# Kernel tuning notes

Hardware: AMD Instinct MI355X
Metric: run time of the kernel (lower is better)

Reference implementation:

```python
import jax, jax.numpy as jnp
import numpy as np
from jax import lax

NUM_BLOCKS = 8
BLOCK = 4  # hidden_size 32 // num_blocks 8
LAMBDA = 0.01  # sparsity_threshold
BN_EPS = 1e-5


def _bn(x, gamma, beta):
    # training-mode BatchNorm2d over (N, H, W) per channel
    mean = jnp.mean(x, axis=(0, 2, 3), keepdims=True)
    var = jnp.var(x, axis=(0, 2, 3), keepdims=True)
    return gamma[None, :, None, None] * (x - mean) * lax.rsqrt(var + BN_EPS) + beta[None, :, None, None]


def _softshrink(x, lam):
    return jnp.where(x > lam, x - lam, jnp.where(x < -lam, x + lam, jnp.zeros_like(x)))


def _afno(x, w1, b1, w2, b2):
    # AFNO2D_channelfirst: rfft2 -> block-diagonal complex 2-layer MLP -> softshrink
    # -> multiply with original spectrum -> irfft2 -> residual add
    B, C, H, W = x.shape
    bias = x
    xf = jnp.fft.rfft2(x, axes=(2, 3), norm="ortho")          # [B, C, H, W//2+1] complex
    orig = xf
    Wf = xf.shape[-1]
    xb = xf.reshape(B, NUM_BLOCKS, BLOCK, H, Wf)
    xr, xi = jnp.real(xb), jnp.imag(xb)
    # layer 1 (complex block matmul + bias + ReLU)
    o1r = jax.nn.relu(jnp.einsum('bkihw,kio->bkohw', xr, w1[0])
                      - jnp.einsum('bkihw,kio->bkohw', xi, w1[1])
                      + b1[0][None, :, :, None, None])
    o1i = jax.nn.relu(jnp.einsum('bkihw,kio->bkohw', xi, w1[0])
                      + jnp.einsum('bkihw,kio->bkohw', xr, w1[1])
                      + b1[1][None, :, :, None, None])
    # layer 2
    o2r = (jnp.einsum('bkihw,kio->bkohw', o1r, w2[0])
           - jnp.einsum('bkihw,kio->bkohw', o1i, w2[1])
           + b2[0][None, :, :, None, None])
    o2i = (jnp.einsum('bkihw,kio->bkohw', o1i, w2[0])
           + jnp.einsum('bkihw,kio->bkohw', o1r, w2[1])
           + b2[1][None, :, :, None, None])
    o2r = _softshrink(o2r, LAMBDA)
    o2i = _softshrink(o2i, LAMBDA)
    z = (o2r + 1j * o2i).reshape(B, C, H, Wf)
    z = z * orig                                              # spectral gating by original spectrum
    out = jnp.fft.irfft2(z, s=(H, W), axes=(2, 3), norm="ortho")
    return out + bias


def setup_inputs() -> dict:
    key = jax.random.key(0)
    ks = jax.random.split(key, 6)
    return {
        "x": jax.random.normal(ks[0], (4, 32, 512, 512), jnp.float32),
        "conv_w": jax.random.normal(ks[1], (32, 32, 3, 3), jnp.float32) * 0.05,
        "conv_b": jnp.zeros((32,), jnp.float32),
        "bn1_gamma": jnp.ones((32,), jnp.float32),
        "bn1_beta": jnp.zeros((32,), jnp.float32),
        "w1": jax.random.normal(ks[2], (2, NUM_BLOCKS, BLOCK, BLOCK), jnp.float32) * 0.02,
        "b1": jax.random.normal(ks[3], (2, NUM_BLOCKS, BLOCK), jnp.float32) * 0.02,
        "w2": jax.random.normal(ks[4], (2, NUM_BLOCKS, BLOCK, BLOCK), jnp.float32) * 0.02,
        "b2": jax.random.normal(ks[5], (2, NUM_BLOCKS, BLOCK), jnp.float32) * 0.02,
        "bn2_gamma": jnp.ones((32,), jnp.float32),
        "bn2_beta": jnp.zeros((32,), jnp.float32),
    }


def reference(x, conv_w, conv_b, bn1_gamma, bn1_beta, w1, b1, w2, b2, bn2_gamma, bn2_beta):
    # conv1 = Conv3x3(norm=True, act=True): conv 3x3 pad 1 + BN + ReLU
    y = lax.conv_general_dilated(x, conv_w, (1, 1), ((1, 1), (1, 1)),
                                 dimension_numbers=('NCHW', 'OIHW', 'NCHW'))
    y = y + conv_b[None, :, None, None]
    y = jax.nn.relu(_bn(y, bn1_gamma, bn1_beta))
    fo = _afno(y, w1, b1, w2, b2)
    fo = _bn(fo, bn2_gamma, bn2_beta)
    return jax.nn.relu(y + fo)
```

## Files before the change

kernel.cpp:

```cpp
#include <hip/hip_runtime.h>

#define WF 257
#define LAM 0.01f
#define ROWH 540
#define LPH(i) ((i) + (((i)>>6)<<2))

#define WSYNC() do { asm volatile("" ::: "memory"); __builtin_amdgcn_wave_barrier(); asm volatile("" ::: "memory"); } while(0)

typedef __attribute__((ext_vector_type(8))) short short8;
typedef __attribute__((ext_vector_type(4))) float f32x4;
typedef __attribute__((ext_vector_type(2))) __fp16 h2v;
typedef __attribute__((ext_vector_type(8))) __fp16 h8;

union UH8 { uint4 u; h8 h; };

__device__ __forceinline__ ushort f2bf(float f){
    unsigned u = __float_as_uint(f);
    unsigned r = (u + 0x7fffu + ((u >> 16) & 1u)) >> 16;
    return (ushort)r;
}
__device__ __forceinline__ float bf2f(ushort u){ return __uint_as_float((uint)u << 16); }
__device__ __forceinline__ uint packbf(float a, float b){
    return (uint)f2bf(a) | ((uint)f2bf(b) << 16);
}
__device__ __forceinline__ float2 unpackbf(uint u){
    return make_float2(__uint_as_float(u << 16), __uint_as_float(u & 0xffff0000u));
}
__device__ __forceinline__ uint packh(float a, float b){
    h2v h;
    h[0] = (__fp16)a;
    h[1] = (__fp16)b;
    return *(uint*)&h;
}
__device__ __forceinline__ uint packh2(float2 v){ return packh(v.x, v.y); }
__device__ __forceinline__ float2 unph(uint u){
    h2v h = *(h2v*)&u;
    return make_float2((float)h[0], (float)h[1]);
}

__device__ __forceinline__ float2 cmul(float2 a, float2 b){
    return make_float2(a.x*b.x - a.y*b.y, a.x*b.y + a.y*b.x);
}
__device__ __forceinline__ float2 cadd(float2 a, float2 b){ return make_float2(a.x+b.x, a.y+b.y); }
__device__ __forceinline__ float2 csub(float2 a, float2 b){ return make_float2(a.x-b.x, a.y-b.y); }

template<int NTHREADS>
__device__ __forceinline__ void ld_tw(float2* tw, const float2* __restrict__ twg, int tid){
    for (int t = tid; t < 256; t += NTHREADS)
        ((float4*)tw)[t] = ((const float4*)twg)[t];
}

template<bool INV>
__device__ __forceinline__ float2 twz(const float2* tw, int idx){
    float2 w = tw[idx];
    if (INV) w.y = -w.y;
    return w;
}

template<bool INV>
__device__ __forceinline__ void dft8(float2 v[8]) {
    const float R = 0.70710678118654752f;
    float2 y0=v[0], y1=v[4], y2=v[2], y3=v[6], y4=v[1], y5=v[5], y6=v[3], y7=v[7];
    float2 t;
    t=y1; y1=csub(y0,t); y0=cadd(y0,t);
    t=y3; y3=csub(y2,t); y2=cadd(y2,t);
    t=y5; y5=csub(y4,t); y4=cadd(y4,t);
    t=y7; y7=csub(y6,t); y6=cadd(y6,t);
    t=y2; y2=csub(y0,t); y0=cadd(y0,t);
    t = INV ? make_float2(-y3.y, y3.x) : make_float2(y3.y, -y3.x);
    y3=csub(y1,t); y1=cadd(y1,t);
    t=y6; y6=csub(y4,t); y4=cadd(y4,t);
    t = INV ? make_float2(-y7.y, y7.x) : make_float2(y7.y, -y7.x);
    y7=csub(y5,t); y5=cadd(y5,t);
    t=y4; y4=csub(y0,t); y0=cadd(y0,t);
    { float2 w8 = INV ? make_float2(R, R) : make_float2(R,-R);
      t=cmul(y5,w8); y5=csub(y1,t); y1=cadd(y1,t); }
    t = INV ? make_float2(-y6.y, y6.x) : make_float2(y6.y, -y6.x);
    y6=csub(y2,t); y2=cadd(y2,t);
    { float2 w8 = INV ? make_float2(-R, R) : make_float2(-R,-R);
      t=cmul(y7,w8); y7=csub(y3,t); y3=cadd(y3,t); }
    v[0]=y0; v[1]=y1; v[2]=y2; v[3]=y3; v[4]=y4; v[5]=y5; v[6]=y6; v[7]=y7;
}

__device__ __forceinline__ void oct_write(uint* drow, int l, const float2 v[8]){
    uint* p = drow + LPH(8*l);
    *(uint4*)p       = make_uint4(packh2(v[0]), packh2(v[1]), packh2(v[2]), packh2(v[3]));
    *(uint4*)(p + 4) = make_uint4(packh2(v[4]), packh2(v[5]), packh2(v[6]), packh2(v[7]));
}

__device__ __forceinline__ void oct_gather(const uint* drow, int o0, float2 v[8]){
    const uint* b = drow + LPH(o0);
    #pragma unroll
    for (int q = 0; q < 8; ++q) v[q] = unph(b[68*q]);
}

template<bool INV>
__device__ __forceinline__ void fft_wave12(uint* drow, const float2* tw, int l)
{
    WSYNC();
    {
        int a = l&7, m = l>>3;
        uint* b = drow + 68*m + a;
        float2 v[8];
        v[0] = unph(b[0]);
        #pragma unroll
        for (int j = 1; j < 8; ++j)
            v[j] = cmul(unph(b[8*j]), twz<INV>(tw, 8*a*j));
        dft8<INV>(v);
        #pragma unroll
        for (int j = 0; j < 8; ++j) b[8*j] = packh2(v[j]);
    }
    WSYNC();
    {
        uint* b = drow + l;
        float2 v[8];
        v[0] = unph(b[0]);
        #pragma unroll
        for (int q = 1; q < 8; ++q)
            v[q] = cmul(unph(b[68*q]), twz<INV>(tw, (l*q)&511));
        dft8<INV>(v);
        #pragma unroll
        for (int q = 0; q < 8; ++q) b[68*q] = packh2(v[q]);
    }
    WSYNC();
}

__global__ void k_twiddle(float2* __restrict__ twg){
    int t = blockIdx.x*256 + threadIdx.x;
    if (t < 512) {
        float s, c;
        sincosf((float)t * (-6.2831853071795864769f/512.0f), &s, &c);
        twg[t] = make_float2(c, s);
    }
}

__device__ __forceinline__ float2 twf(int idx){
    float s, c;
    sincosf((float)(idx & 511) * (-6.2831853071795864769f/512.0f), &s, &c);
    return make_float2(c, s);
}

__global__ void k_mfrag(uint4* __restrict__ fA, uint4* __restrict__ fB,
                        uint4* __restrict__ fG, uint4* __restrict__ fC)
{
    const int lane = threadIdx.x;
    const int bx = blockIdx.x;
    const int l15 = lane & 15;
    const int kb = (lane >> 4) * 8;
    if (bx < 2) {
        const int mt = bx;
        const int m = mt*16 + l15;
        uint ur[4], ui[4], un[4];
        for (int p = 0; p < 4; ++p) {
            float2 t0 = twf(16*m*(kb + 2*p));
            float2 t1 = twf(16*m*(kb + 2*p+1));
            ur[p] = packh(t0.x, t1.x);
            ui[p] = packh(t0.y, t1.y);
            un[p] = ui[p] ^ 0x80008000u;
        }
        fA[(lane*2 + mt)*3 + 0] = make_uint4(ur[0],ur[1],ur[2],ur[3]);
        fA[(lane*2 + mt)*3 + 1] = make_uint4(ui[0],ui[1],ui[2],ui[3]);
        fA[(lane*2 + mt)*3 + 2] = make_uint4(un[0],un[1],un[2],un[3]);
    } else if (bx < 34) {
        const int k2 = bx - 2;
        uint ar[4]={0,0,0,0}, ai[4]={0,0,0,0}, an[4]={0,0,0,0};
        if (lane < 32) {
            const int kk = k2 + 32*l15;
            for (int p = 0; p < 4; ++p) {
                float2 t0 = twf((kb + 2*p)*kk);
                float2 t1 = twf((kb + 2*p+1)*kk);
                ar[p] = packh(t0.x, t1.x);
                ai[p] = packh(t0.y, t1.y);
                an[p] = ai[p] ^ 0x80008000u;
            }
        }
        fB[(lane*32 + k2)*3 + 0] = make_uint4(ar[0],ar[1],ar[2],ar[3]);
        fB[(lane*32 + k2)*3 + 1] = make_uint4(ai[0],ai[1],ai[2],ai[3]);
        fB[(lane*32 + k2)*3 + 2] = make_uint4(an[0],an[1],an[2],an[3]);
    } else if (bx == 34) {
        uint gr[4]={0,0,0,0}, gi[4]={0,0,0,0}, gn[4]={0,0,0,0};
        if (lane < 32) {
            for (int p = 0; p < 4; ++p) {
                float2 t0 = twf(32*(kb + 2*p)*l15);
                float2 t1 = twf(32*(kb + 2*p+1)*l15);
                gr[p] = packh(t0.x, t1.x);
                gi[p] = packh(-t0.y, -t1.y);
                gn[p] = gi[p] ^ 0x80008000u;
            }
        }
        fG[lane*3 + 0] = make_uint4(gr[0],gr[1],gr[2],gr[3]);
        fG[lane*3 + 1] = make_uint4(gi[0],gi[1],gi[2],gi[3]);
        fG[lane*3 + 2] = make_uint4(gn[0],gn[1],gn[2],gn[3]);
    } else {
        const int t = bx - 35;
        const int n1 = t >> 1, mt = t & 1;
        const int hh = n1 + 16*(mt*16 + l15);
        uint cr[4], ci[4], cn[4];
        for (int p = 0; p < 4; ++p) {
            float2 t0 = twf(hh*(kb + 2*p));
            float2 t1 = twf(hh*(kb + 2*p+1));
            cr[p] = packh(t0.x, t1.x);
            ci[p] = packh(-t0.y, -t1.y);
            cn[p] = ci[p] ^ 0x80008000u;
        }
        fC[((lane*16 + n1)*2 + mt)*3 + 0] = make_uint4(cr[0],cr[1],cr[2],cr[3]);
        fC[((lane*16 + n1)*2 + mt)*3 + 1] = make_uint4(ci[0],ci[1],ci[2],ci[3]);
        fC[((lane*16 + n1)*2 + mt)*3 + 2] = make_uint4(cn[0],cn[1],cn[2],cn[3]);
    }
}

__global__ void k_wprep(const float* __restrict__ w, ushort* __restrict__ wtp){
    int i = blockIdx.x*256 + threadIdx.x;
    if (i < 9216) {
        int j = i & 7, l = (i>>3) & 63, m = (i>>9) & 1, tap = i >> 10;
        int co = m*16 + (l & 15), ci = ((l>>4)&3)*8 + j;
        wtp[i] = f2bf(w[(co*32 + ci)*9 + tap]);
    }
}

__global__ __launch_bounds__(256) void k_transpose(const float* __restrict__ x, ushort* __restrict__ xt){
    __shared__ ushort tl[64][36];
    const int tid = threadIdx.x;
    const int w0 = blockIdx.x*64, h = blockIdx.y, b = blockIdx.z;
    #pragma unroll
    for (int it = 0; it < 8; ++it) {
        int i = it*256 + tid, c = i >> 6, ww = i & 63;
        tl[ww][c] = f2bf(x[(((size_t)b*32 + c)*512 + h)*512 + w0 + ww]);
    }
    __syncthreads();
    const int ww = tid >> 2, c0 = (tid & 3) * 8;
    uint4 v;
    v.x = *(const uint*)&tl[ww][c0+0];
    v.y = *(const uint*)&tl[ww][c0+2];
    v.z = *(const uint*)&tl[ww][c0+4];
    v.w = *(const uint*)&tl[ww][c0+6];
    *(uint4*)(xt + ((((size_t)b*512 + h)*512 + w0 + ww)*32 + c0)) = v;
}

__global__ __launch_bounds__(256) void k_conv_mfma(
    const ushort* __restrict__ xt, const ushort* __restrict__ wtp,
    const float* __restrict__ bias, ushort* __restrict__ out, float* __restrict__ stats)
{
    __shared__ float sred[64];
    const int tid = threadIdx.x;
    const int wid = tid >> 6, lane = tid & 63;
    const int h = blockIdx.y*4 + wid;
    const int w0 = blockIdx.x*64;
    const int b = blockIdx.z;

    short8 wa[9][2];
    #pragma unroll
    for (int tap = 0; tap < 9; ++tap)
        #pragma unroll
        for (int m = 0; m < 2; ++m)
            wa[tap][m] = *reinterpret_cast<const short8*>(wtp + ((tap*2 + m)*64 + lane)*8);

    f32x4 acc[2][4];
    #pragma unroll
    for (int m = 0; m < 2; ++m)
        #pragma unroll
        for (int n = 0; n < 4; ++n)
            acc[m][n] = (f32x4){0.f, 0.f, 0.f, 0.f};

    const int c0 = ((lane >> 4) & 3) * 8;
    const int pw = w0 + (lane & 15);
    const size_t ibase = (size_t)b * 512 * 512;

    #pragma unroll
    for (int dy = -1; dy <= 1; ++dy) {
        const int hh = h + dy;
        const bool hok = (unsigned)hh < 512u;
        #pragma unroll
        for (int dx = -1; dx <= 1; ++dx) {
            const int tap = (dy+1)*3 + (dx+1);
            short8 bfr[4];
            #pragma unroll
            for (int n = 0; n < 4; ++n) {
                const int ww = pw + n*16 + dx;
                short8 v = {0,0,0,0,0,0,0,0};
                if (hok && (unsigned)ww < 512u)
                    v = *reinterpret_cast<const short8*>(xt + ((ibase + (size_t)hh*512 + ww)*32 + c0));
                bfr[n] = v;
            }
            #pragma unroll
            for (int m = 0; m < 2; ++m)
                #pragma unroll
                for (int n = 0; n < 4; ++n)
                    acc[m][n] = __builtin_amdgcn_mfma_f32_16x16x32_bf16(wa[tap][m], bfr[n], acc[m][n], 0, 0, 0);
        }
    }

    if (tid < 64) sred[tid] = 0.f;
    __syncthreads();

    float bv[2][4];
    #pragma unroll
    for (int m = 0; m < 2; ++m)
        #pragma unroll
        for (int r = 0; r < 4; ++r)
            bv[m][r] = bias[m*16 + ((lane>>4)&3)*4 + r];

    float s8[8], q8[8];
    #pragma unroll
    for (int i = 0; i < 8; ++i) { s8[i] = 0.f; q8[i] = 0.f; }

    #pragma unroll
    for (int m = 0; m < 2; ++m) {
        #pragma unroll
        for (int n = 0; n < 4; ++n) {
            #pragma unroll
            for (int r = 0; r < 4; ++r) {
                const int co = m*16 + ((lane>>4)&3)*4 + r;
                const int ww = w0 + n*16 + (lane & 15);
                float val = acc[m][n][r] + bv[m][r];
                out[(((size_t)b*32 + co)*512 + h)*512 + ww] = f2bf(val);
                s8[m*4+r] += val;
                q8[m*4+r] += val*val;
            }
        }
    }
    #pragma unroll
    for (int i = 0; i < 8; ++i) {
        #pragma unroll
        for (int off = 1; off < 16; off <<= 1) {
            s8[i] += __shfl_xor(s8[i], off, 64);
            q8[i] += __shfl_xor(q8[i], off, 64);
        }
    }
    if ((lane & 15) == 0) {
        #pragma unroll
        for (int m = 0; m < 2; ++m)
            #pragma unroll
            for (int r = 0; r < 4; ++r) {
                const int co = m*16 + ((lane>>4)&3)*4 + r;
                atomicAdd(&sred[co], s8[m*4+r]);
                atomicAdd(&sred[32+co], q8[m*4+r]);
            }
    }
    __syncthreads();
    if (tid < 64) {
        int bin = (blockIdx.y*8 + blockIdx.x + blockIdx.z) & 63;
        atomicAdd(&stats[bin*64 + tid], sred[tid]);
    }
}

__global__ void k_finalize(const float* __restrict__ stats, int nbins, const float* __restrict__ g,
                           const float* __restrict__ bta, float* __restrict__ bnp)
{
    int c = threadIdx.x;
    if (c < 32) {
        float s = 0.f, q = 0.f;
        for (int i = 0; i < nbins; ++i) { s += stats[i*64 + c]; q += stats[i*64 + 32 + c]; }
        const float inv_n = 1.f/1048576.f;
        float mean = s * inv_n;
        float var  = q * inv_n - mean*mean;
        float sc = g[c] * rsqrtf(var + 1e-5f);
        bnp[c] = sc;
        bnp[32+c] = bta[c] - mean*sc;
    }
}

__global__ void k_finalize2(const float* __restrict__ ystats, const float* __restrict__ sstats,
                            const float* __restrict__ g, const float* __restrict__ bta,
                            float* __restrict__ bnp2)
{
    int c = threadIdx.x;
    if (c < 32) {
        float Sy = 0.f, Sy2 = 0.f, Sgg = 0.f, Sgu = 0.f, Sg0 = 0.f;
        for (int i = 0; i < 64; ++i){ Sy  += ystats[i*64 + c]; Sy2 += ystats[i*64 + 32 + c]; }
        for (int i = 0; i < 32; ++i){ Sgg += sstats[i*96 + c]; Sgu += sstats[i*96 + 32 + c]; Sg0 += sstats[i*96 + 64 + c]; }
        const float inv_n = 1.f/1048576.f;
        float Sfo  = Sg0 + Sy;
        float Sfo2 = Sgg*(1.f/512.f) + Sgu*(2.f/512.f) + Sy2;
        float mean = Sfo*inv_n;
        float var  = Sfo2*inv_n - mean*mean;
        float sc = g[c]*rsqrtf(var + 1e-5f);
        bnp2[c] = sc;
        bnp2[32+c] = bta[c] - mean*sc;
    }
}

__global__ __launch_bounds__(512) void k_rowfft_fwd(
    const ushort* __restrict__ cvo, const float* __restrict__ bnp,
    const float2* __restrict__ twg, uint* __restrict__ spec, float* __restrict__ ystats)
{
    __shared__ float2 tw[512];
    __shared__ uint d[8*ROWH];
    const int tid = threadIdx.x;
    const int h0 = blockIdx.x * 16;
    const int bc = blockIdx.y;
    const int c = bc & 31;
    ld_tw<512>(tw, twg, tid);
    __syncthreads();
    const float s1 = bnp[c], t1 = bnp[32+c];
    const int row = tid >> 6, l = tid & 63;
    const int o0 = ((l&7)<<3) | (l>>3);
    uint* drow = d + row*ROWH;
    const ushort* rp0 = cvo + ((size_t)bc*512 + h0 + 2*row)*512 + o0;
    const ushort* rp1 = rp0 + 512;
    float ls = 0.f, lsq = 0.f;
    float2 v[8];
    #pragma unroll
    for (int q = 0; q < 8; ++q) {
        float y0 = fmaxf(fmaf(bf2f(rp0[64*q]), s1, t1), 0.f);
        float y1 = fmaxf(fmaf(bf2f(rp1[64*q]), s1, t1), 0.f);
        ls += y0 + y1; lsq += y0*y0 + y1*y1;
        v[q] = make_float2(y0, y1);
    }
    dft8<false>(v);
    oct_write(drow, l, v);
    fft_wave12<false>(drow, tw, l);
    __syncthreads();
    for (int i = tid; i < 8*WF; i += 512) {
        int p = i & 7, w = i >> 3;
        float2 Z  = unph(d[p*ROWH + LPH(w)]);
        float2 Zm = unph(d[p*ROWH + LPH((512 - w) & 511)]);
        float x1r = 0.5f*(Z.x + Zm.x), x1i = 0.5f*(Z.y - Zm.y);
        float x2r = 0.5f*(Z.y + Zm.y), x2i = 0.5f*(Zm.x - Z.x);
        uint2 pk;
        pk.x = packbf(x1r, x1i);
        pk.y = packbf(x2r, x2i);
        *(uint2*)(spec + ((size_t)bc*WF + w)*512 + h0 + 2*p) = pk;
    }
    #pragma unroll
    for (int off = 32; off; off >>= 1){ ls += __shfl_down(ls, off, 64); lsq += __shfl_down(lsq, off, 64); }
    if (l == 0) {
        int bin = ((blockIdx.x << 3) + row) & 63;
        atomicAdd(&ystats[bin*64 + c], ls);
        atomicAdd(&ystats[bin*64 + 32 + c], lsq);
    }
}

__global__ __launch_bounds__(512) void k_colfft(uint* __restrict__ spec,
    const float* __restrict__ w1, const float* __restrict__ b1,
    const float* __restrict__ w2, const float* __restrict__ b2,
    const uint4* __restrict__ fA, const uint4* __restrict__ fB,
    const uint4* __restrict__ fG, const uint4* __restrict__ fC,
    float* __restrict__ sstats)
{
    __shared__ uint sl[32*513];
    __shared__ float wl[640];
    const int tid = threadIdx.x;
    const int lane = tid & 63, wv = tid >> 6;
    const int w = blockIdx.x, b = blockIdx.y;
    const int l15 = lane & 15, lq = lane >> 4;
    const int kb = lq * 8;

    if (tid < 128) {
        int g = tid >> 4, j = tid & 15;
        wl[g*80 + j]      = w1[g*16 + j];
        wl[g*80 + 16 + j] = w1[128 + g*16 + j];
        wl[g*80 + 32 + j] = w2[g*16 + j];
        wl[g*80 + 48 + j] = w2[128 + g*16 + j];
    } else if (tid < 160) {
        int t2 = tid - 128, g = t2 >> 2, o = t2 & 3;
        wl[g*80 + 64 + o] = b1[g*4 + o];
        wl[g*80 + 68 + o] = b1[32 + g*4 + o];
        wl[g*80 + 72 + o] = b2[g*4 + o];
        wl[g*80 + 76 + o] = b2[32 + g*4 + o];
    }
    const size_t gbase = ((size_t)b*32*WF + w) * 512;
    #pragma unroll 4
    for (int c = 0; c < 32; ++c) {
        float2 u = unpackbf(spec[gbase + (size_t)c*(WF*512) + tid]);
        sl[c*513 + tid] = packh(u.x*(1.f/512.f), u.y*(1.f/512.f));
    }
    __syncthreads();

    {
        h8 Fr[2], Fi[2], nFi[2];
        #pragma unroll
        for (int mt = 0; mt < 2; ++mt) {
            UH8 a; a.u = fA[(lane*2 + mt)*3 + 0]; Fr[mt]=a.h;
            UH8 bb; bb.u = fA[(lane*2 + mt)*3 + 1]; Fi[mt]=bb.h;
            UH8 cc; cc.u = fA[(lane*2 + mt)*3 + 2]; nFi[mt]=cc.h;
        }
        #pragma unroll
        for (int s = 0; s < 2; ++s) {
            const int n1 = wv*2 + s;
            h8 Br[2], Bi[2];
            #pragma unroll
            for (int nt = 0; nt < 2; ++nt) {
                const int base = (nt*16 + l15)*513 + n1;
                uint dd[8];
                #pragma unroll
                for (int j = 0; j < 8; ++j) dd[j] = sl[base + 16*(kb + j)];
                uint br[4], bi[4];
                #pragma unroll
                for (int p = 0; p < 4; ++p) {
                    br[p] = (dd[2*p] & 0xffffu) | (dd[2*p+1] << 16);
                    bi[p] = (dd[2*p] >> 16) | (dd[2*p+1] & 0xffff0000u);
                }
                UH8 t1_; t1_.u = make_uint4(br[0],br[1],br[2],br[3]); Br[nt]=t1_.h;
                UH8 t2_; t2_.u = make_uint4(bi[0],bi[1],bi[2],bi[3]); Bi[nt]=t2_.h;
            }
            __builtin_amdgcn_s_setprio(1);
            #pragma unroll
            for (int mt = 0; mt < 2; ++mt)
            #pragma unroll
            for (int nt = 0; nt < 2; ++nt) {
                f32x4 yr = {0.f,0.f,0.f,0.f}, yi = {0.f,0.f,0.f,0.f};
                yr = __builtin_amdgcn_mfma_f32_16x16x32_f16(Fr[mt], Br[nt], yr, 0,0,0);
                yr = __builtin_amdgcn_mfma_f32_16x16x32_f16(nFi[mt], Bi[nt], yr, 0,0,0);
                yi = __builtin_amdgcn_mfma_f32_16x16x32_f16(Fr[mt], Bi[nt], yi, 0,0,0);
                yi = __builtin_amdgcn_mfma_f32_16x16x32_f16(Fi[mt], Br[nt], yi, 0,0,0);
                const int cw = (nt*16 + l15)*513 + n1;
                #pragma unroll
                for (int r = 0; r < 4; ++r)
                    sl[cw + 16*(mt*16 + lq*4 + r)] = packh(yr[r], yi[r]);
            }
            __builtin_amdgcn_s_setprio(0);
        }
    }
    __syncthreads();

    #pragma unroll
    for (int s = 0; s < 4; ++s) {
        const int k2 = wv*4 + s;
        h8 Ar, Ai, nAi;
        {
            UH8 a; a.u = fB[(lane*32 + k2)*3 + 0]; Ar=a.h;
            UH8 bb; bb.u = fB[(lane*32 + k2)*3 + 1]; Ai=bb.h;
            UH8 cc; cc.u = fB[(lane*32 + k2)*3 + 2]; nAi=cc.h;
        }
        #pragma unroll
        for (int ct = 0; ct < 2; ++ct) {
            const int cb2 = (ct*16 + l15)*513 + 16*k2;
            h8 Br, Bi;
            {
                uint dd[8] = {0,0,0,0,0,0,0,0};
                if (lane < 32) {
                    #pragma unroll
                    for (int j = 0; j < 8; ++j) dd[j] = sl[cb2 + kb + j];
                }
                uint br[4], bi[4];
                #pragma unroll
                for (int p = 0; p < 4; ++p) {
                    br[p] = (dd[2*p] & 0xffffu) | (dd[2*p+1] << 16);
                    bi[p] = (dd[2*p] >> 16) | (dd[2*p+1] & 0xffff0000u);
                }
                UH8 t1_; t1_.u = make_uint4(br[0],br[1],br[2],br[3]); Br=t1_.h;
                UH8 t2_; t2_.u = make_uint4(bi[0],bi[1],bi[2],bi[3]); Bi=t2_.h;
            }
            __builtin_amdgcn_s_setprio(1);
            f32x4 xr = {0.f,0.f,0.f,0.f}, xi = {0.f,0.f,0.f,0.f};
            xr = __builtin_amdgcn_mfma_f32_16x16x32_f16(Ar, Br, xr, 0,0,0);
            xr = __builtin_amdgcn_mfma_f32_16x16x32_f16(nAi, Bi, xr, 0,0,0);
            xi = __builtin_amdgcn_mfma_f32_16x16x32_f16(Ar, Bi, xi, 0,0,0);
            xi = __builtin_amdgcn_mfma_f32_16x16x32_f16(Ai, Br, xi, 0,0,0);
            __builtin_amdgcn_s_setprio(0);
            #pragma unroll
            for (int r = 0; r < 4; ++r)
                sl[cb2 + lq*4 + r] = packh(xr[r], xi[r]);
        }
    }
    __syncthreads();

    #pragma unroll
    for (int g = 0; g < 8; ++g) {
        const float* wk = wl + g*80;
        float xr[4], xi[4];
        #pragma unroll
        for (int i = 0; i < 4; ++i) {
            float2 v = unph(sl[(4*g+i)*513 + tid]);
            xr[i] = v.x; xi[i] = v.y;
        }
        float o1r[4], o1i[4];
        #pragma unroll
        for (int o = 0; o < 4; ++o) {
            float sr = wk[64+o], si = wk[68+o];
            #pragma unroll
            for (int i = 0; i < 4; ++i) {
                float wr = wk[i*4+o], wi = wk[16 + i*4+o];
                sr += xr[i]*wr - xi[i]*wi;
                si += xi[i]*wr + xr[i]*wi;
            }
            o1r[o] = fmaxf(sr, 0.f);
            o1i[o] = fmaxf(si, 0.f);
        }
        #pragma unroll
        for (int o = 0; o < 4; ++o) {
            float sr = wk[72+o], si = wk[76+o];
            #pragma unroll
            for (int i = 0; i < 4; ++i) {
                float wr = wk[32 + i*4+o], wi = wk[48 + i*4+o];
                sr += o1r[i]*wr - o1i[i]*wi;
                si += o1i[i]*wr + o1r[i]*wi;
            }
            sr = (sr > LAM) ? sr - LAM : ((sr < -LAM) ? sr + LAM : 0.f);
            si = (si > LAM) ? si - LAM : ((si < -LAM) ? si + LAM : 0.f);
            sl[(4*g+o)*513 + tid] = packh(sr*xr[o] - si*xi[o], sr*xi[o] + si*xr[o]);
        }
    }
    __syncthreads();

    {
        h8 Gr, Gi, nGi;
        {
            UH8 a; a.u = fG[lane*3 + 0]; Gr=a.h;
            UH8 bb; bb.u = fG[lane*3 + 1]; Gi=bb.h;
            UH8 cc; cc.u = fG[lane*3 + 2]; nGi=cc.h;
        }
        #pragma unroll
        for (int s = 0; s < 4; ++s) {
            const int k2 = wv*4 + s;
            #pragma unroll
            for (int ct = 0; ct < 2; ++ct) {
                const int cb2 = (ct*16 + l15)*513 + 16*k2;
                h8 Br, Bi;
                {
                    uint dd[8] = {0,0,0,0,0,0,0,0};
                    if (lane < 32) {
                        #pragma unroll
                        for (int j = 0; j < 8; ++j) dd[j] = sl[cb2 + kb + j];
                    }
                    uint br[4], bi[4];
                    #pragma unroll
                    for (int p = 0; p < 4; ++p) {
                        br[p] = (dd[2*p] & 0xffffu) | (dd[2*p+1] << 16);
                        bi[p] = (dd[2*p] >> 16) | (dd[2*p+1] & 0xffff0000u);
                    }
                    UH8 t1_; t1_.u = make_uint4(br[0],br[1],br[2],br[3]); Br=t1_.h;
                    UH8 t2_; t2_.u = make_uint4(bi[0],bi[1],bi[2],bi[3]); Bi=t2_.h;
                }
                __builtin_amdgcn_s_setprio(1);
                f32x4 yr = {0.f,0.f,0.f,0.f}, yi = {0.f,0.f,0.f,0.f};
                yr = __builtin_amdgcn_mfma_f32_16x16x32_f16(Gr, Br, yr, 0,0,0);
                yr = __builtin_amdgcn_mfma_f32_16x16x32_f16(nGi, Bi, yr, 0,0,0);
                yi = __builtin_amdgcn_mfma_f32_16x16x32_f16(Gr, Bi, yi, 0,0,0);
                yi = __builtin_amdgcn_mfma_f32_16x16x32_f16(Gi, Br, yi, 0,0,0);
                __builtin_amdgcn_s_setprio(0);
                #pragma unroll
                for (int r = 0; r < 4; ++r)
                    sl[cb2 + lq*4 + r] = packh(yr[r], yi[r]);
            }
        }
    }
    __syncthreads();

    #pragma unroll
    for (int s = 0; s < 2; ++s) {
        const int n1 = wv*2 + s;
        h8 Cr[2], Ci[2], nCi[2];
        #pragma unroll
        for (int mt = 0; mt < 2; ++mt) {
            UH8 a; a.u = fC[((lane*16 + n1)*2 + mt)*3 + 0]; Cr[mt]=a.h;
            UH8 bb; bb.u = fC[((lane*16 + n1)*2 + mt)*3 + 1]; Ci[mt]=bb.h;
            UH8 cc; cc.u = fC[((lane*16 + n1)*2 + mt)*3 + 2]; nCi[mt]=cc.h;
        }
        h8 Br[2], Bi[2];
        #pragma unroll
        for (int nt = 0; nt < 2; ++nt) {
            const int base = (nt*16 + l15)*513 + n1;
            uint dd[8];
            #pragma unroll
            for (int j = 0; j < 8; ++j) dd[j] = sl[base + 16*(kb + j)];
            uint br[4], bi[4];
            #pragma unroll
            for (int p = 0; p < 4; ++p) {
                br[p] = (dd[2*p] & 0xffffu) | (dd[2*p+1] << 16);
                bi[p] = (dd[2*p] >> 16) | (dd[2*p+1] & 0xffff0000u);
            }
            UH8 t1_; t1_.u = make_uint4(br[0],br[1],br[2],br[3]); Br[nt]=t1_.h;
            UH8 t2_; t2_.u = make_uint4(bi[0],bi[1],bi[2],bi[3]); Bi[nt]=t2_.h;
        }
        __builtin_amdgcn_s_setprio(1);
        #pragma unroll
        for (int mt = 0; mt < 2; ++mt)
        #pragma unroll
        for (int nt = 0; nt < 2; ++nt) {
            f32x4 xr = {0.f,0.f,0.f,0.f}, xi = {0.f,0.f,0.f,0.f};
            xr = __builtin_amdgcn_mfma_f32_16x16x32_f16(Cr[mt], Br[nt], xr, 0,0,0);
            xr = __builtin_amdgcn_mfma_f32_16x16x32_f16(nCi[mt], Bi[nt], xr, 0,0,0);
            xi = __builtin_amdgcn_mfma_f32_16x16x32_f16(Cr[mt], Bi[nt], xi, 0,0,0);
            xi = __builtin_amdgcn_mfma_f32_16x16x32_f16(Ci[mt], Br[nt], xi, 0,0,0);
            const int cw = (nt*16 + l15)*513 + n1;
            #pragma unroll
            for (int r = 0; r < 4; ++r)
                sl[cw + 16*(mt*16 + lq*4 + r)] = packh(xr[r], xi[r]);
        }
        __builtin_amdgcn_s_setprio(0);
    }
    __syncthreads();

    const bool edge = (w == 0) || (w == 256);
    #pragma unroll
    for (int i = 0; i < 4; ++i) {
        const int c = wv*4 + i;
        const size_t cb = gbase + (size_t)c*(WF*512);
        float fgg = 0.f, fgu = 0.f, fg0 = 0.f;
        #pragma unroll
        for (int it = 0; it < 4; ++it) {
            const int pos = it*128 + 2*lane;
            uint2 dv;
            dv.x = sl[c*513 + pos];
            dv.y = sl[c*513 + pos + 1];
            float2 z0 = unph(dv.x), z1 = unph(dv.y);
            uint2 up = *(const uint2*)(spec + cb + pos);
            float2 u0 = unpackbf(up.x), u1 = unpackbf(up.y);
            uint2 gp;
            gp.x = packbf(z0.x, z0.y);
            gp.y = packbf(z1.x, z1.y);
            *(uint2*)(spec + cb + pos) = gp;
            float2 g0 = unpackbf(gp.x), g1 = unpackbf(gp.y);
            if (edge) {
                fgg += g0.x*g0.x + g1.x*g1.x;
                fgu += g0.x*u0.x + g1.x*u1.x;
                if (w == 0) fg0 += g0.x + g1.x;
            } else {
                fgg += 2.f*(g0.x*g0.x + g0.y*g0.y + g1.x*g1.x + g1.y*g1.y);
                fgu += 2.f*(g0.x*u0.x + g0.y*u0.y + g1.x*u1.x + g1.y*u1.y);
            }
        }
        #pragma unroll
        for (int off = 32; off; off >>= 1){
            fgg += __shfl_down(fgg, off, 64);
            fgu += __shfl_down(fgu, off, 64);
            fg0 += __shfl_down(fg0, off, 64);
        }
        if (lane == 0) {
            const int kk = c >> 2, ch = c & 3;
            const int bin = (w + b*8 + kk) & 31;
            atomicAdd(&sstats[bin*96 + kk*4 + ch], fgg);
            atomicAdd(&sstats[bin*96 + 32 + kk*4 + ch], fgu);
            if (w == 0) atomicAdd(&sstats[bin*96 + 64 + kk*4 + ch], fg0);
        }
    }
}

__global__ __launch_bounds__(512) void k_rowfft_inv(
    const uint* __restrict__ spec, const ushort* __restrict__ cvo,
    const float* __restrict__ bnp, const float* __restrict__ bnp2,
    const float2* __restrict__ twg, float* __restrict__ out)
{
    __shared__ float2 tw[512];
    __shared__ uint d[8*ROWH];
    const int tid = threadIdx.x;
    const int h0 = blockIdx.x * 16;
    const int bc = blockIdx.y;
    const int c = bc & 31;
    ld_tw<512>(tw, twg, tid);
    for (int i = tid; i < 8*WF; i += 512) {
        int p = i & 7, w = i >> 3;
        uint2 pk = *(const uint2*)(spec + ((size_t)bc*WF + w)*512 + h0 + 2*p);
        float2 X1 = unpackbf(pk.x), X2 = unpackbf(pk.y);
        if (w == 0 || w == 256) { X1.y = 0.f; X2.y = 0.f; }
        const float s = 1.f/512.f;
        d[p*ROWH + LPH(w)] = packh((X1.x - X2.y)*s, (X1.y + X2.x)*s);
        if ((unsigned)(w - 1) < 255u)
            d[p*ROWH + LPH(512 - w)] = packh((X1.x + X2.y)*s, (X2.x - X1.y)*s);
    }
    __syncthreads();
    const int row = tid >> 6, l = tid & 63;
    const int o0 = ((l&7)<<3) | (l>>3);
    uint* drow = d + row*ROWH;
    {
        float2 v[8];
        oct_gather(drow, o0, v);
        dft8<true>(v);
        WSYNC();
        oct_write(drow, l, v);
    }
    fft_wave12<true>(drow, tw, l);
    const float s1 = bnp[c],  t1 = bnp[32+c];
    const float s2 = bnp2[c], t2 = bnp2[32+c];
    const size_t gbase = ((size_t)bc*512 + h0 + 2*row)*512;
    #pragma unroll
    for (int q = 0; q < 8; ++q) {
        const int col = q*64 + l;
        float2 v = unph(drow[LPH(col)]);
        float y0 = fmaxf(fmaf(bf2f(cvo[gbase + col]), s1, t1), 0.f);
        float fo0 = v.x + y0;
        out[gbase + col] = fmaxf(y0 + fmaf(fo0, s2, t2), 0.f);
        float y1 = fmaxf(fmaf(bf2f(cvo[gbase + 512 + col]), s1, t1), 0.f);
        float fo1 = v.y + y1;
        out[gbase + 512 + col] = fmaxf(y1 + fmaf(fo1, s2, t2), 0.f);
    }
}

extern "C" void kernel_launch(void* const* d_in, const int* in_sizes, int n_in,
                              void* d_out, int out_size, void* d_ws, size_t ws_size,
                              hipStream_t stream)
{
    const float* x      = (const float*)d_in[0];
    const float* conv_w = (const float*)d_in[1];
    const float* conv_b = (const float*)d_in[2];
    const float* bn1g   = (const float*)d_in[3];
    const float* bn1b   = (const float*)d_in[4];
    const float* w1     = (const float*)d_in[5];
    const float* b1     = (const float*)d_in[6];
    const float* w2     = (const float*)d_in[7];
    const float* b2     = (const float*)d_in[8];
    const float* bn2g   = (const float*)d_in[9];
    const float* bn2b   = (const float*)d_in[10];
    float* out = (float*)d_out;

    char* ws = (char*)d_ws;
    uint*   spec  = (uint*)ws;
    ushort* xt    = (ushort*)ws;
    ushort* cvo   = (ushort*)(ws + 67371008);
    ushort* wtp   = (ushort*)(ws + 67371008 + 67108864);
    float*  stats = (float*)(ws + 67371008 + 67108864 + 18432);
    float* stats1 = stats;
    float* ystats = stats + 4096;
    float* sstats = stats + 8192;
    float* bnp1   = stats + 11264;
    float* bnp2   = stats + 11328;
    float2* twg   = (float2*)(stats + 11392);
    uint4* fA = (uint4*)(stats + 12416);
    uint4* fB = fA + 384;
    uint4* fG = fB + 6144;
    uint4* fC = fG + 192;

    (void)hipMemsetAsync(stats, 0, 11264*sizeof(float), stream);
    k_twiddle<<<2, 256, 0, stream>>>(twg);
    k_mfrag<<<67, 64, 0, stream>>>(fA, fB, fG, fC);
    k_wprep<<<36, 256, 0, stream>>>(conv_w, wtp);
    k_transpose<<<dim3(8,512,4), 256, 0, stream>>>(x, xt);
    k_conv_mfma<<<dim3(8,128,4), 256, 0, stream>>>(xt, wtp, conv_b, cvo, stats1);
    k_finalize<<<1, 64, 0, stream>>>(stats1, 64, bn1g, bn1b, bnp1);
    k_rowfft_fwd<<<dim3(32,128), 512, 0, stream>>>(cvo, bnp1, twg, spec, ystats);
    k_colfft<<<dim3(257,4), 512, 0, stream>>>(spec, w1, b1, w2, b2, fA, fB, fG, fC, sstats);
    k_finalize2<<<1, 64, 0, stream>>>(ystats, sstats, bn2g, bn2b, bnp2);
    k_rowfft_inv<<<dim3(32,128), 512, 0, stream>>>(spec, cvo, bnp1, bnp2, twg, out);
}
```

Measured before the change: 327.7 us.

## Split column FFT kernel across two channel halves to double block count

The column-FFT/spectral-MLP kernel now processes 16 channels per block instead of 32, with a third grid dimension selecting the channel half. Launching 2056 blocks instead of 1028 halves shared memory per block (about 33KB), which should allow more resident blocks per CU and better latency hiding. The cost is that per-block setup such as loading DFT fragments and weights is repeated, and each wave now does less MFMA work per fragment load.

```diff
diff --git a/kernel.cpp b/kernel.cpp
--- a/kernel.cpp
+++ b/kernel.cpp
@@ -438,30 +438,32 @@
     const uint4* __restrict__ fG, const uint4* __restrict__ fC,
     float* __restrict__ sstats)
 {
-    __shared__ uint sl[32*513];
-    __shared__ float wl[640];
+    __shared__ uint sl[16*513];
+    __shared__ float wl[320];
     const int tid = threadIdx.x;
     const int lane = tid & 63, wv = tid >> 6;
-    const int w = blockIdx.x, b = blockIdx.y;
+    const int w = blockIdx.x, b = blockIdx.y, half = blockIdx.z;
     const int l15 = lane & 15, lq = lane >> 4;
     const int kb = lq * 8;
 
-    if (tid < 128) {
+    if (tid < 64) {
         int g = tid >> 4, j = tid & 15;
-        wl[g*80 + j]      = w1[g*16 + j];
-        wl[g*80 + 16 + j] = w1[128 + g*16 + j];
-        wl[g*80 + 32 + j] = w2[g*16 + j];
-        wl[g*80 + 48 + j] = w2[128 + g*16 + j];
-    } else if (tid < 160) {
-        int t2 = tid - 128, g = t2 >> 2, o = t2 & 3;
-        wl[g*80 + 64 + o] = b1[g*4 + o];
-        wl[g*80 + 68 + o] = b1[32 + g*4 + o];
-        wl[g*80 + 72 + o] = b2[g*4 + o];
-        wl[g*80 + 76 + o] = b2[32 + g*4 + o];
-    }
-    const size_t gbase = ((size_t)b*32*WF + w) * 512;
+        int gg = half*4 + g;
+        wl[g*80 + j]      = w1[gg*16 + j];
+        wl[g*80 + 16 + j] = w1[128 + gg*16 + j];
+        wl[g*80 + 32 + j] = w2[gg*16 + j];
+        wl[g*80 + 48 + j] = w2[128 + gg*16 + j];
+    } else if (tid < 80) {
+        int t2 = tid - 64, g = t2 >> 2, o = t2 & 3;
+        int gg = half*4 + g;
+        wl[g*80 + 64 + o] = b1[gg*4 + o];
+        wl[g*80 + 68 + o] = b1[32 + gg*4 + o];
+        wl[g*80 + 72 + o] = b2[gg*4 + o];
+        wl[g*80 + 76 + o] = b2[32 + gg*4 + o];
+    }
+    const size_t gbase = ((size_t)(b*32 + half*16)*WF + w) * 512;
     #pragma unroll 4
-    for (int c = 0; c < 32; ++c) {
+    for (int c = 0; c < 16; ++c) {
         float2 u = unpackbf(spec[gbase + (size_t)c*(WF*512) + tid]);
         sl[c*513 + tid] = packh(u.x*(1.f/512.f), u.y*(1.f/512.f));
     }
@@ -478,10 +480,9 @@
         #pragma unroll
         for (int s = 0; s < 2; ++s) {
             const int n1 = wv*2 + s;
-            h8 Br[2], Bi[2];
-            #pragma unroll
-            for (int nt = 0; nt < 2; ++nt) {
-                const int base = (nt*16 + l15)*513 + n1;
+            h8 Br, Bi;
+            {
+                const int base = l15*513 + n1;
                 uint dd[8];
                 #pragma unroll
                 for (int j = 0; j < 8; ++j) dd[j] = sl[base + 16*(kb + j)];
@@ -491,20 +492,18 @@
                     br[p] = (dd[2*p] & 0xffffu) | (dd[2*p+1] << 16);
                     bi[p] = (dd[2*p] >> 16) | (dd[2*p+1] & 0xffff0000u);
                 }
-                UH8 t1_; t1_.u = make_uint4(br[0],br[1],br[2],br[3]); Br[nt]=t1_.h;
-                UH8 t2_; t2_.u = make_uint4(bi[0],bi[1],bi[2],bi[3]); Bi[nt]=t2_.h;
+                UH8 t1_; t1_.u = make_uint4(br[0],br[1],br[2],br[3]); Br=t1_.h;
+                UH8 t2_; t2_.u = make_uint4(bi[0],bi[1],bi[2],bi[3]); Bi=t2_.h;
             }
             __builtin_amdgcn_s_setprio(1);
             #pragma unroll
-            for (int mt = 0; mt < 2; ++mt)
-            #pragma unroll
-            for (int nt = 0; nt < 2; ++nt) {
+            for (int mt = 0; mt < 2; ++mt) {
                 f32x4 yr = {0.f,0.f,0.f,0.f}, yi = {0.f,0.f,0.f,0.f};
-                yr = __builtin_amdgcn_mfma_f32_16x16x32_f16(Fr[mt], Br[nt], yr, 0,0,0);
-                yr = __builtin_amdgcn_mfma_f32_16x16x32_f16(nFi[mt], Bi[nt], yr, 0,0,0);
-                yi = __builtin_amdgcn_mfma_f32_16x16x32_f16(Fr[mt], Bi[nt], yi, 0,0,0);
-                yi = __builtin_amdgcn_mfma_f32_16x16x32_f16(Fi[mt], Br[nt], yi, 0,0,0);
-                const int cw = (nt*16 + l15)*513 + n1;
+                yr = __builtin_amdgcn_mfma_f32_16x16x32_f16(Fr[mt], Br, yr, 0,0,0);
+                yr = __builtin_amdgcn_mfma_f32_16x16x32_f16(nFi[mt], Bi, yr, 0,0,0);
+                yi = __builtin_amdgcn_mfma_f32_16x16x32_f16(Fr[mt], Bi, yi, 0,0,0);
+                yi = __builtin_amdgcn_mfma_f32_16x16x32_f16(Fi[mt], Br, yi, 0,0,0);
+                const int cw = l15*513 + n1;
                 #pragma unroll
                 for (int r = 0; r < 4; ++r)
                     sl[cw + 16*(mt*16 + lq*4 + r)] = packh(yr[r], yi[r]);
@@ -523,9 +522,85 @@
             UH8 bb; bb.u = fB[(lane*32 + k2)*3 + 1]; Ai=bb.h;
             UH8 cc; cc.u = fB[(lane*32 + k2)*3 + 2]; nAi=cc.h;
         }
-        #pragma unroll
-        for (int ct = 0; ct < 2; ++ct) {
-            const int cb2 = (ct*16 + l15)*513 + 16*k2;
+        const int cb2 = l15*513 + 16*k2;
+        h8 Br, Bi;
+        {
+            uint dd[8] = {0,0,0,0,0,0,0,0};
+            if (lane < 32) {
+                #pragma unroll
+                for (int j = 0; j < 8; ++j) dd[j] = sl[cb2 + kb + j];
+            }
+            uint br[4], bi[4];
+            #pragma unroll
+            for (int p = 0; p < 4; ++p) {
+                br[p] = (dd[2*p] & 0xffffu) | (dd[2*p+1] << 16);
+                bi[p] = (dd[2*p] >> 16) | (dd[2*p+1] & 0xffff0000u);
+            }
+            UH8 t1_; t1_.u = make_uint4(br[0],br[1],br[2],br[3]); Br=t1_.h;
+            UH8 t2_; t2_.u = make_uint4(bi[0],bi[1],bi[2],bi[3]); Bi=t2_.h;
+        }
+        __builtin_amdgcn_s_setprio(1);
+        f32x4 xr = {0.f,0.f,0.f,0.f}, xi = {0.f,0.f,0.f,0.f};
+        xr = __builtin_amdgcn_mfma_f32_16x16x32_f16(Ar, Br, xr, 0,0,0);
+        xr = __builtin_amdgcn_mfma_f32_16x16x32_f16(nAi, Bi, xr, 0,0,0);
+        xi = __builtin_amdgcn_mfma_f32_16x16x32_f16(Ar, Bi, xi, 0,0,0);
+        xi = __builtin_amdgcn_mfma_f32_16x16x32_f16(Ai, Br, xi, 0,0,0);
+        __builtin_amdgcn_s_setprio(0);
+        #pragma unroll
+        for (int r = 0; r < 4; ++r)
+            sl[cb2 + lq*4 + r] = packh(xr[r], xi[r]);
+    }
+    __syncthreads();
+
+    #pragma unroll
+    for (int g = 0; g < 4; ++g) {
+        const float* wk = wl + g*80;
+        float xr[4], xi[4];
+        #pragma unroll
+        for (int i = 0; i < 4; ++i) {
+            float2 v = unph(sl[(4*g+i)*513 + tid]);
+            xr[i] = v.x; xi[i] = v.y;
+        }
+        float o1r[4], o1i[4];
+        #pragma unroll
+        for (int o = 0; o < 4; ++o) {
+            float sr = wk[64+o], si = wk[68+o];
+            #pragma unroll
+            for (int i = 0; i < 4; ++i) {
+                float wr = wk[i*4+o], wi = wk[16 + i*4+o];
+                sr += xr[i]*wr - xi[i]*wi;
+                si += xi[i]*wr + xr[i]*wi;
+            }
+            o1r[o] = fmaxf(sr, 0.f);
+            o1i[o] = fmaxf(si, 0.f);
+        }
+        #pragma unroll
+        for (int o = 0; o < 4; ++o) {
+            float sr = wk[72+o], si = wk[76+o];
+            #pragma unroll
+            for (int i = 0; i < 4; ++i) {
+                float wr = wk[32 + i*4+o], wi = wk[48 + i*4+o];
+                sr += o1r[i]*wr - o1i[i]*wi;
+                si += o1i[i]*wr + o1r[i]*wi;
+            }
+            sr = (sr > LAM) ? sr - LAM : ((sr < -LAM) ? sr + LAM : 0.f);
+            si = (si > LAM) ? si - LAM : ((si < -LAM) ? si + LAM : 0.f);
+            sl[(4*g+o)*513 + tid] = packh(sr*xr[o] - si*xi[o], sr*xi[o] + si*xr[o]);
+        }
+    }
+    __syncthreads();
+
+    {
+        h8 Gr, Gi, nGi;
+        {
+            UH8 a; a.u = fG[lane*3 + 0]; Gr=a.h;
+            UH8 bb; bb.u = fG[lane*3 + 1]; Gi=bb.h;
+            UH8 cc; cc.u = fG[lane*3 + 2]; nGi=cc.h;
+        }
+        #pragma unroll
+        for (int s = 0; s < 4; ++s) {
+            const int k2 = wv*4 + s;
+            const int cb2 = l15*513 + 16*k2;
             h8 Br, Bi;
             {
                 uint dd[8] = {0,0,0,0,0,0,0,0};
@@ -543,97 +618,15 @@
                 UH8 t2_; t2_.u = make_uint4(bi[0],bi[1],bi[2],bi[3]); Bi=t2_.h;
             }
             __builtin_amdgcn_s_setprio(1);
-            f32x4 xr = {0.f,0.f,0.f,0.f}, xi = {0.f,0.f,0.f,0.f};
-            xr = __builtin_amdgcn_mfma_f32_16x16x32_f16(Ar, Br, xr, 0,0,0);
-            xr = __builtin_amdgcn_mfma_f32_16x16x32_f16(nAi, Bi, xr, 0,0,0);
-            xi = __builtin_amdgcn_mfma_f32_16x16x32_f16(Ar, Bi, xi, 0,0,0);
-            xi = __builtin_amdgcn_mfma_f32_16x16x32_f16(Ai, Br, xi, 0,0,0);
+            f32x4 yr = {0.f,0.f,0.f,0.f}, yi = {0.f,0.f,0.f,0.f};
+            yr = __builtin_amdgcn_mfma_f32_16x16x32_f16(Gr, Br, yr, 0,0,0);
+            yr = __builtin_amdgcn_mfma_f32_16x16x32_f16(nGi, Bi, yr, 0,0,0);
+            yi = __builtin_amdgcn_mfma_f32_16x16x32_f16(Gr, Bi, yi, 0,0,0);
+            yi = __builtin_amdgcn_mfma_f32_16x16x32_f16(Gi, Br, yi, 0,0,0);
             __builtin_amdgcn_s_setprio(0);
             #pragma unroll
             for (int r = 0; r < 4; ++r)
-                sl[cb2 + lq*4 + r] = packh(xr[r], xi[r]);
-        }
-    }
-    __syncthreads();
-
-    #pragma unroll
-    for (int g = 0; g < 8; ++g) {
-        const float* wk = wl + g*80;
-        float xr[4], xi[4];
-        #pragma unroll
-        for (int i = 0; i < 4; ++i) {
-            float2 v = unph(sl[(4*g+i)*513 + tid]);
-            xr[i] = v.x; xi[i] = v.y;
-        }
-        float o1r[4], o1i[4];
-        #pragma unroll
-        for (int o = 0; o < 4; ++o) {
-            float sr = wk[64+o], si = wk[68+o];
-            #pragma unroll
-            for (int i = 0; i < 4; ++i) {
-                float wr = wk[i*4+o], wi = wk[16 + i*4+o];
-                sr += xr[i]*wr - xi[i]*wi;
-                si += xi[i]*wr + xr[i]*wi;
-            }
-            o1r[o] = fmaxf(sr, 0.f);
-            o1i[o] = fmaxf(si, 0.f);
-        }
-        #pragma unroll
-        for (int o = 0; o < 4; ++o) {
-            float sr = wk[72+o], si = wk[76+o];
-            #pragma unroll
-            for (int i = 0; i < 4; ++i) {
-                float wr = wk[32 + i*4+o], wi = wk[48 + i*4+o];
-                sr += o1r[i]*wr - o1i[i]*wi;
-                si += o1i[i]*wr + o1r[i]*wi;
-            }
-            sr = (sr > LAM) ? sr - LAM : ((sr < -LAM) ? sr + LAM : 0.f);
-            si = (si > LAM) ? si - LAM : ((si < -LAM) ? si + LAM : 0.f);
-            sl[(4*g+o)*513 + tid] = packh(sr*xr[o] - si*xi[o], sr*xi[o] + si*xr[o]);
-        }
-    }
-    __syncthreads();
-
-    {
-        h8 Gr, Gi, nGi;
-        {
-            UH8 a; a.u = fG[lane*3 + 0]; Gr=a.h;
-            UH8 bb; bb.u = fG[lane*3 + 1]; Gi=bb.h;
-            UH8 cc; cc.u = fG[lane*3 + 2]; nGi=cc.h;
-        }
-        #pragma unroll
-        for (int s = 0; s < 4; ++s) {
-            const int k2 = wv*4 + s;
-            #pragma unroll
-            for (int ct = 0; ct < 2; ++ct) {
-                const int cb2 = (ct*16 + l15)*513 + 16*k2;
-                h8 Br, Bi;
-                {
-                    uint dd[8] = {0,0,0,0,0,0,0,0};
-                    if (lane < 32) {
-                        #pragma unroll
-                        for (int j = 0; j < 8; ++j) dd[j] = sl[cb2 + kb + j];
-                    }
-                    uint br[4], bi[4];
-                    #pragma unroll
-                    for (int p = 0; p < 4; ++p) {
-                        br[p] = (dd[2*p] & 0xffffu) | (dd[2*p+1] << 16);
-                        bi[p] = (dd[2*p] >> 16) | (dd[2*p+1] & 0xffff0000u);
-                    }
-                    UH8 t1_; t1_.u = make_uint4(br[0],br[1],br[2],br[3]); Br=t1_.h;
-                    UH8 t2_; t2_.u = make_uint4(bi[0],bi[1],bi[2],bi[3]); Bi=t2_.h;
-                }
-                __builtin_amdgcn_s_setprio(1);
-                f32x4 yr = {0.f,0.f,0.f,0.f}, yi = {0.f,0.f,0.f,0.f};
-                yr = __builtin_amdgcn_mfma_f32_16x16x32_f16(Gr, Br, yr, 0,0,0);
-                yr = __builtin_amdgcn_mfma_f32_16x16x32_f16(nGi, Bi, yr, 0,0,0);
-                yi = __builtin_amdgcn_mfma_f32_16x16x32_f16(Gr, Bi, yi, 0,0,0);
-                yi = __builtin_amdgcn_mfma_f32_16x16x32_f16(Gi, Br, yi, 0,0,0);
-                __builtin_amdgcn_s_setprio(0);
-                #pragma unroll
-                for (int r = 0; r < 4; ++r)
-                    sl[cb2 + lq*4 + r] = packh(yr[r], yi[r]);
-            }
+                sl[cb2 + lq*4 + r] = packh(yr[r], yi[r]);
         }
     }
     __syncthreads();
@@ -648,10 +641,9 @@
             UH8 bb; bb.u = fC[((lane*16 + n1)*2 + mt)*3 + 1]; Ci[mt]=bb.h;
             UH8 cc; cc.u = fC[((lane*16 + n1)*2 + mt)*3 + 2]; nCi[mt]=cc.h;
         }
-        h8 Br[2], Bi[2];
-        #pragma unroll
-        for (int nt = 0; nt < 2; ++nt) {
-            const int base = (nt*16 + l15)*513 + n1;
+        h8 Br, Bi;
+        {
+            const int base = l15*513 + n1;
             uint dd[8];
             #pragma unroll
             for (int j = 0; j < 8; ++j) dd[j] = sl[base + 16*(kb + j)];
@@ -661,20 +653,18 @@
                 br[p] = (dd[2*p] & 0xffffu) | (dd[2*p+1] << 16);
                 bi[p] = (dd[2*p] >> 16) | (dd[2*p+1] & 0xffff0000u);
             }
-            UH8 t1_; t1_.u = make_uint4(br[0],br[1],br[2],br[3]); Br[nt]=t1_.h;
-            UH8 t2_; t2_.u = make_uint4(bi[0],bi[1],bi[2],bi[3]); Bi[nt]=t2_.h;
+            UH8 t1_; t1_.u = make_uint4(br[0],br[1],br[2],br[3]); Br=t1_.h;
+            UH8 t2_; t2_.u = make_uint4(bi[0],bi[1],bi[2],bi[3]); Bi=t2_.h;
         }
         __builtin_amdgcn_s_setprio(1);
         #pragma unroll
-        for (int mt = 0; mt < 2; ++mt)
-        #pragma unroll
-        for (int nt = 0; nt < 2; ++nt) {
+        for (int mt = 0; mt < 2; ++mt) {
             f32x4 xr = {0.f,0.f,0.f,0.f}, xi = {0.f,0.f,0.f,0.f};
-            xr = __builtin_amdgcn_mfma_f32_16x16x32_f16(Cr[mt], Br[nt], xr, 0,0,0);
-            xr = __builtin_amdgcn_mfma_f32_16x16x32_f16(nCi[mt], Bi[nt], xr, 0,0,0);
-            xi = __builtin_amdgcn_mfma_f32_16x16x32_f16(Cr[mt], Bi[nt], xi, 0,0,0);
-            xi = __builtin_amdgcn_mfma_f32_16x16x32_f16(Ci[mt], Br[nt], xi, 0,0,0);
-            const int cw = (nt*16 + l15)*513 + n1;
+            xr = __builtin_amdgcn_mfma_f32_16x16x32_f16(Cr[mt], Br, xr, 0,0,0);
+            xr = __builtin_amdgcn_mfma_f32_16x16x32_f16(nCi[mt], Bi, xr, 0,0,0);
+            xi = __builtin_amdgcn_mfma_f32_16x16x32_f16(Cr[mt], Bi, xi, 0,0,0);
+            xi = __builtin_amdgcn_mfma_f32_16x16x32_f16(Ci[mt], Br, xi, 0,0,0);
+            const int cw = l15*513 + n1;
             #pragma unroll
             for (int r = 0; r < 4; ++r)
                 sl[cw + 16*(mt*16 + lq*4 + r)] = packh(xr[r], xi[r]);
@@ -685,16 +675,17 @@
 
     const bool edge = (w == 0) || (w == 256);
     #pragma unroll
-    for (int i = 0; i < 4; ++i) {
-        const int c = wv*4 + i;
-        const size_t cb = gbase + (size_t)c*(WF*512);
+    for (int i = 0; i < 2; ++i) {
+        const int cl = wv*2 + i;
+        const int cg = half*16 + cl;
+        const size_t cb = gbase + (size_t)cl*(WF*512);
         float fgg = 0.f, fgu = 0.f, fg0 = 0.f;
         #pragma unroll
         for (int it = 0; it < 4; ++it) {
             const int pos = it*128 + 2*lane;
             uint2 dv;
-            dv.x = sl[c*513 + pos];
-            dv.y = sl[c*513 + pos + 1];
+            dv.x = sl[cl*513 + pos];
+            dv.y = sl[cl*513 + pos + 1];
             float2 z0 = unph(dv.x), z1 = unph(dv.y);
             uint2 up = *(const uint2*)(spec + cb + pos);
             float2 u0 = unpackbf(up.x), u1 = unpackbf(up.y);
@@ -719,7 +710,7 @@
             fg0 += __shfl_down(fg0, off, 64);
         }
         if (lane == 0) {
-            const int kk = c >> 2, ch = c & 3;
+            const int kk = cg >> 2, ch = cg & 3;
             const int bin = (w + b*8 + kk) & 31;
             atomicAdd(&sstats[bin*96 + kk*4 + ch], fgg);
             atomicAdd(&sstats[bin*96 + 32 + kk*4 + ch], fgu);
@@ -820,7 +811,7 @@
     k_conv_mfma<<<dim3(8,128,4), 256, 0, stream>>>(xt, wtp, conv_b, cvo, stats1);
     k_finalize<<<1, 64, 0, stream>>>(stats1, 64, bn1g, bn1b, bnp1);
     k_rowfft_fwd<<<dim3(32,128), 512, 0, stream>>>(cvo, bnp1, twg, spec, ystats);
-    k_colfft<<<dim3(257,4), 512, 0, stream>>>(spec, w1, b1, w2, b2, fA, fB, fG, fC, sstats);
+    k_colfft<<<dim3(257,4,2), 512, 0, stream>>>(spec, w1, b1, w2, b2, fA, fB, fG, fC, sstats);
     k_finalize2<<<1, 64, 0, stream>>>(ystats, sstats, bn2g, bn2b, bnp2);
     k_rowfft_inv<<<dim3(32,128), 512, 0, stream>>>(spec, cvo, bnp1, bnp2, twg, out);
 }
```

Result: slower. 375.3 us (+14.5%).
